# Optimization experiments

Measured on AMD Instinct MI355X. Metric: run time of the kernel, lower is better.

## Reference

```python
import jax, jax.numpy as jnp
import numpy as np

B, T, D, H = 256, 1024, 64, 512
I = 1 + D          # time channel + data
O = 2 * D          # mean + std
STD_LB = 1e-3


def setup_inputs() -> dict:
    key = jax.random.key(0)
    ks = jax.random.split(key, 8)
    s = 0.05  # small init scale
    return {
        "xs": jax.random.normal(ks[0], (B, T, D), jnp.float32),
        "ts": jax.random.uniform(ks[1], (B, T, 1), jnp.float32),
        "W_ih": jax.random.normal(ks[2], (3 * H, I), jnp.float32) * s,
        "W_hh": jax.random.normal(ks[3], (3 * H, H), jnp.float32) * s,
        "b_ih": jax.random.normal(ks[4], (3 * H,), jnp.float32) * s,
        "b_hh": jax.random.normal(ks[5], (3 * H,), jnp.float32) * s,
        "W_dec": jax.random.normal(ks[6], (O, H), jnp.float32) * s,
        "b_dec": jax.random.normal(ks[7], (O,), jnp.float32) * s,
        "cutoff": 512,  # int(inference_start * seq_len) with inference_start=0.5
    }


def reference(xs, ts, W_ih, W_hh, b_ih, b_hh, W_dec, b_dec, cutoff):
    b, t_len, d = xs.shape
    h_dim = W_hh.shape[1]

    def step(carry, inp):
        h, x_hat = carry
        x_true, t_curr, t_idx = inp
        force = t_idx < cutoff  # teacher forcing for t < cutoff
        x_t = jnp.where(force, x_true, x_hat)                 # (B, D)
        x_in = jnp.concatenate([t_curr[:, :1], x_t], axis=-1)  # (B, 1+D)
        gi = x_in @ W_ih.T + b_ih                              # (B, 3H)
        gh = h @ W_hh.T + b_hh                                 # (B, 3H)
        i_r, i_z, i_n = jnp.split(gi, 3, axis=-1)
        h_r, h_z, h_n = jnp.split(gh, 3, axis=-1)
        r = jax.nn.sigmoid(i_r + h_r)
        z = jax.nn.sigmoid(i_z + h_z)
        n = jnp.tanh(i_n + r * h_n)
        h_new = (1.0 - z) * n + z * h                          # GRUCell update
        dec = h_new @ W_dec.T + b_dec                          # (B, 2D)
        mean = dec[:, :d]
        std = jnp.maximum(dec[:, d:], STD_LB)                  # clamp(min=std_lower_bound)
        out = jnp.concatenate([mean, std], axis=-1)
        return (h_new, mean), out

    h0 = jnp.zeros((b, h_dim), xs.dtype)
    init = (h0, xs[:, 0, :])
    xs_t = jnp.swapaxes(xs, 0, 1)   # (T, B, D)
    ts_t = jnp.swapaxes(ts, 0, 1)   # (T, B, 1)
    t_idx = jnp.arange(t_len)
    _, outs = jax.lax.scan(step, init, (xs_t, ts_t, t_idx))
    return jnp.swapaxes(outs, 0, 1)  # (B, T, 2D)
```

## Files before the change

kernel.cpp:

```cpp
#include <hip/hip_runtime.h>
#include <hip/hip_bf16.h>
#include <cstdint>
#include <cstddef>

typedef float f32x4 __attribute__((ext_vector_type(4)));
typedef short s16x8 __attribute__((ext_vector_type(8)));

#define B_  256
#define T_  1024
#define D_  64
#define H_  512
#define O_  128
#define JW  16
#define NG  48

#define SLABW64 49152

#define OFF_WGH   0
#define OFF_WGI2  49152
#define OFF_WGIX  98304
#define OFF_WDEC  104448
#define OFF_W0S   120832
#define OFF_C0S   121024
#define OFF_BIHS  121216
#define OFF_BHHS  121408
#define OFF_BDECS 121600
#define OFF_SCR   121728
#define OFF_SCRF  122752
#define SMEM_BYTES 124928

#define WS_WCOMB 0
#define WS_C0    1572864
#define WS_HSLAB 1579008
#define WS_HSZ   786432

__device__ inline f32x4 mfma16(s16x8 a, s16x8 b, f32x4 c) {
  return __builtin_amdgcn_mfma_f32_16x16x32_bf16(a, b, c, 0, 0, 0);
}

__device__ inline unsigned short f2bf(float f) {
  __hip_bfloat16 h = __float2bfloat16(f);
  unsigned short u;
  __builtin_memcpy(&u, &h, sizeof(u));
  return u;
}

__device__ inline s16x8 cvt8(const float* s) {
  union { unsigned short h[8]; s16x8 v; } p;
#pragma unroll
  for (int e = 0; e < 8; ++e) p.h[e] = f2bf(s[e]);
  return p.v;
}

__device__ inline s16x8 fragK512(const char* base, int n, int kc, int kg) {
  int byteoff = n * 1024 + (((kc * 64) + (kg * 16)) ^ ((n & 7) << 4));
  return *(const s16x8*)(base + byteoff);
}
__device__ inline s16x8 fragK64(const char* base, int n, int kc, int kg) {
  int byteoff = n * 128 + (((kc * 64) + (kg * 16)) ^ ((n & 7) << 4));
  return *(const s16x8*)(base + byteoff);
}

__device__ inline unsigned long long ld64a(const unsigned long long* p) {
  return __hip_atomic_load(p, __ATOMIC_RELAXED, __HIP_MEMORY_SCOPE_AGENT);
}
__device__ inline void st64a(unsigned long long* p, unsigned long long v) {
  __hip_atomic_store(p, v, __ATOMIC_RELAXED, __HIP_MEMORY_SCOPE_AGENT);
}

__device__ inline s16x8 unpack3(unsigned long long w0, unsigned long long w1,
                                unsigned long long w2) {
  union { unsigned short u[8]; s16x8 v; } ua;
  ua.u[0] = (unsigned short)w0; ua.u[1] = (unsigned short)(w0 >> 16);
  ua.u[2] = (unsigned short)(w0 >> 32);
  ua.u[3] = (unsigned short)w1; ua.u[4] = (unsigned short)(w1 >> 16);
  ua.u[5] = (unsigned short)(w1 >> 32);
  ua.u[6] = (unsigned short)w2; ua.u[7] = (unsigned short)(w2 >> 16);
  return ua.v;
}

#define LOADG8(W, KC0)                                                    \
  {                                                                       \
    _Pragma("unroll") for (int k_ = 0; k_ < 8; ++k_) {                    \
      W[k_ * 3 + 0] = ld64a(rqL + ((KC0) + k_) * 192 + 0);                \
      W[k_ * 3 + 1] = ld64a(rqL + ((KC0) + k_) * 192 + 1);                \
      W[k_ * 3 + 2] = ld64a(rqL + ((KC0) + k_) * 192 + 2);                \
    }                                                                     \
  }

#define VERIFY8(W, KC0)                                                   \
  {                                                                       \
    for (;;) {                                                            \
      unsigned long long bad_ = 0;                                        \
      _Pragma("unroll") for (int i_ = 0; i_ < 24; ++i_)                   \
          bad_ |= (W[i_] >> 48) ^ tge;                                    \
      if (!__any((int)(bad_ != 0))) break;                                \
      if (--budget <= 0) break;                                           \
      LOADG8(W, KC0)                                                      \
    }                                                                     \
  }

#define UNPACKG8(W, KC0)                                                  \
  {                                                                       \
    _Pragma("unroll") for (int k_ = 0; k_ < 8; ++k_)                      \
        a[(KC0) + k_] =                                                   \
            unpack3(W[k_ * 3], W[k_ * 3 + 1], W[k_ * 3 + 2]);             \
  }

__global__ void wcomb_kernel(const float* __restrict__ W_ih, const float* __restrict__ W_dec,
                             const float* __restrict__ b_ih, const float* __restrict__ b_dec,
                             unsigned short* __restrict__ Wcomb, float* __restrict__ c0) {
  __shared__ float arow[64];
  int i = blockIdx.x;
  int tid = threadIdx.x;
  if (tid < 64) arow[tid] = W_ih[(size_t)i * 65 + 1 + tid];
  __syncthreads();
  for (int j = tid; j < H_; j += 256) {
    float acc = 0.f;
#pragma unroll 8
    for (int d = 0; d < 64; ++d) acc += arow[d] * W_dec[(size_t)d * H_ + j];
    Wcomb[(size_t)i * H_ + j] = f2bf(acc);
  }
  if (tid == 0) {
    float acc = b_ih[i];
    for (int d = 0; d < 64; ++d) acc += arow[d] * b_dec[d];
    c0[i] = acc;
  }
}

__global__ __launch_bounds__(128, 1) void rnn_persist(
    const float* __restrict__ xs, const float* __restrict__ ts,
    const float* __restrict__ W_ih, const float* __restrict__ W_hh,
    const float* __restrict__ b_ih, const float* __restrict__ b_hh,
    const float* __restrict__ W_dec, const float* __restrict__ b_dec,
    const int* __restrict__ cutoffp,
    const unsigned short* __restrict__ Wcomb, const float* __restrict__ c0,
    unsigned long long* __restrict__ hslabE, float* __restrict__ out) {
  extern __shared__ char sm[];
  const int tid = threadIdx.x;
  const int wave = tid >> 6, lane = tid & 63;
  const int jl = lane & 15, kg = lane >> 4;
  const int cutoff = *cutoffp;

  const int bg = blockIdx.x & 7;
  const int cg = blockIdx.x >> 3;
  const int b0 = bg * 32;
  const int j0 = cg * JW;

  for (int u = tid; u < NG * 64; u += 128) {
    int r = u >> 6, blk = u & 63;
    int grow = (r >> 4) * H_ + j0 + (r & 15);
    s16x8 v = cvt8(W_hh + (size_t)grow * H_ + blk * 8);
    *(s16x8*)(sm + OFF_WGH + r * 1024 + ((blk * 16) ^ ((r & 7) << 4))) = v;
  }
  for (int u = tid; u < NG * 64; u += 128) {
    int r = u >> 6, blk = u & 63;
    int grow = (r >> 4) * H_ + j0 + (r & 15);
    s16x8 v = *(const s16x8*)(Wcomb + (size_t)grow * H_ + blk * 8);
    *(s16x8*)(sm + OFF_WGI2 + r * 1024 + ((blk * 16) ^ ((r & 7) << 4))) = v;
  }
  for (int u = tid; u < NG * 8; u += 128) {
    int r = u >> 3, blk = u & 7;
    int grow = (r >> 4) * H_ + j0 + (r & 15);
    s16x8 v = cvt8(W_ih + (size_t)grow * 65 + 1 + blk * 8);
    *(s16x8*)(sm + OFF_WGIX + r * 128 + ((blk * 16) ^ ((r & 7) << 4))) = v;
  }
  if (cg >= 24) {
    for (int u = tid; u < 16 * 64; u += 128) {
      int r = u >> 6, blk = u & 63;
      s16x8 v = cvt8(W_dec + (size_t)((cg - 24) * 16 + r) * H_ + blk * 8);
      *(s16x8*)(sm + OFF_WDEC + r * 1024 + ((blk * 16) ^ ((r & 7) << 4))) = v;
    }
    if (tid < 16) ((float*)(sm + OFF_BDECS))[tid] = b_dec[(cg - 24) * 16 + tid];
  }
  if (tid < NG) {
    int grow = (tid >> 4) * H_ + j0 + (tid & 15);
    ((float*)(sm + OFF_W0S))[tid]  = W_ih[(size_t)grow * 65];
    ((float*)(sm + OFF_C0S))[tid]  = c0[grow];
    ((float*)(sm + OFF_BIHS))[tid] = b_ih[grow];
    ((float*)(sm + OFF_BHHS))[tid] = b_hh[grow];
  }
  __syncthreads();

  const int mt = wave;
  const int rowg = b0 + mt * 16 + jl;
  const int hrow = b0 + mt * 16 + kg * 4;
  unsigned short* scr = (unsigned short*)(sm + OFF_SCR) + mt * 256;
  float* scrF = (float*)(sm + OFF_SCRF) + mt * 272;
  int budget = 200000;

  const size_t blkb = (size_t)(bg * 2 + mt) * 3072;
  const size_t laneoff = (size_t)kg * 48 + (size_t)jl * 3;
  const int wi0 = lane;
  const int wr0 = wi0 / 6, wk0 = wi0 % 6;
  const int wi1 = 64 + lane;
  const int wr1 = wi1 / 6, wk1 = wi1 % 6;

  const float* W0S  = (const float*)(sm + OFF_W0S);
  const float* C0S  = (const float*)(sm + OFF_C0S);
  const float* BIHS = (const float*)(sm + OFF_BIHS);
  const float* BHHS = (const float*)(sm + OFF_BHHS);
  const float w0r = W0S[jl],  w0z = W0S[16 + jl],  w0n = W0S[32 + jl];
  const float bir = BIHS[jl], biz = BIHS[16 + jl], bin_ = BIHS[32 + jl];
  const float c0r = C0S[jl],  c0z = C0S[16 + jl],  c0n = C0S[32 + jl];
  const float bhr = BHHS[jl], bhz = BHHS[16 + jl], bhn = BHHS[32 + jl];

  const bool do_dec = (cg >= 24);
  const float bd = do_dec ? ((const float*)(sm + OFF_BDECS))[jl] : 0.f;

  float hp[4] = {0.f, 0.f, 0.f, 0.f};
  s16x8 a[16];

  for (int t = 0; t < T_; ++t) {
    const bool use_x = (t < cutoff) || (t == 0);
    const unsigned long long tge = (unsigned long long)(unsigned)t;
    const unsigned long long epw = (unsigned long long)(t + 1) << 48;
    const unsigned long long* rqL =
        hslabE + (size_t)((t + 1) & 1) * SLABW64 + blkb + laneoff;
    unsigned long long* wq = hslabE + (size_t)(t & 1) * SLABW64 + blkb;

    float tsv[4];
#pragma unroll
    for (int reg = 0; reg < 4; ++reg) tsv[reg] = ts[(size_t)(hrow + reg) * T_ + t];

    f32x4 g0{}, g1{}, g2{}, i0{}, i1{}, i2{};
    if (use_x) {
      s16x8 ax0 = cvt8(xs + ((size_t)rowg * T_ + t) * D_ + kg * 8);
      s16x8 ax1 = cvt8(xs + ((size_t)rowg * T_ + t) * D_ + 32 + kg * 8);
      i0 = mfma16(ax0, fragK64(sm + OFF_WGIX, jl,      0, kg), i0);
      i1 = mfma16(ax0, fragK64(sm + OFF_WGIX, 16 + jl, 0, kg), i1);
      i2 = mfma16(ax0, fragK64(sm + OFF_WGIX, 32 + jl, 0, kg), i2);
      i0 = mfma16(ax1, fragK64(sm + OFF_WGIX, jl,      1, kg), i0);
      i1 = mfma16(ax1, fragK64(sm + OFF_WGIX, 16 + jl, 1, kg), i1);
      i2 = mfma16(ax1, fragK64(sm + OFF_WGIX, 32 + jl, 1, kg), i2);
    }

    if (t > 0) {
      unsigned long long wA[24], wB[24];

#define MFMA_CL8(K0)                                                         \
      { _Pragma("unroll") for (int k_ = 0; k_ < 8; ++k_) {                   \
          int kc_ = (K0) + k_;                                               \
          g0 = mfma16(a[kc_], fragK512(sm + OFF_WGH, jl,      kc_, kg), g0); \
          g1 = mfma16(a[kc_], fragK512(sm + OFF_WGH, 16 + jl, kc_, kg), g1); \
          g2 = mfma16(a[kc_], fragK512(sm + OFF_WGH, 32 + jl, kc_, kg), g2); \
          if (!use_x) {                                                      \
            i0 = mfma16(a[kc_], fragK512(sm + OFF_WGI2, jl,      kc_, kg), i0); \
            i1 = mfma16(a[kc_], fragK512(sm + OFF_WGI2, 16 + jl, kc_, kg), i1); \
            i2 = mfma16(a[kc_], fragK512(sm + OFF_WGI2, 32 + jl, kc_, kg), i2); \
          } } }

      LOADG8(wA, 0)
      VERIFY8(wA, 0)
      LOADG8(wB, 8)
      UNPACKG8(wA, 0)
      MFMA_CL8(0)
      VERIFY8(wB, 8)
      UNPACKG8(wB, 8)
      MFMA_CL8(8)
#undef MFMA_CL8
    }

    unsigned short hb[4];
#pragma unroll
    for (int reg = 0; reg < 4; ++reg) {
      const float xr = i0[reg] + tsv[reg] * w0r + (use_x ? bir : c0r) + g0[reg] + bhr;
      const float xz = i1[reg] + tsv[reg] * w0z + (use_x ? biz : c0z) + g1[reg] + bhz;
      const float an = i2[reg] + tsv[reg] * w0n + (use_x ? bin_ : c0n);
      const float gn = g2[reg] + bhn;
      const float r = 1.f / (1.f + __expf(-xr));
      const float z = 1.f / (1.f + __expf(-xz));
      const float e2 = __expf(2.f * (an + r * gn));
      const float n = 1.f - 2.f / (e2 + 1.f);
      const float hn = (1.f - z) * n + z * hp[reg];
      hp[reg] = hn;
      hb[reg] = f2bf(hn);
    }

#pragma unroll
    for (int reg = 0; reg < 4; ++reg) scr[(kg * 4 + reg) * 16 + jl] = hb[reg];
    asm volatile("s_waitcnt lgkmcnt(0)" ::: "memory");
    __builtin_amdgcn_sched_barrier(0);
    {
      const int fg = wk0 / 3, pos = wk0 % 3;
      const int cb = fg * 8 + pos * 3;
      unsigned long long v =
          (unsigned long long)scr[wr0 * 16 + cb] |
          ((unsigned long long)scr[wr0 * 16 + cb + 1] << 16) |
          (pos < 2 ? ((unsigned long long)scr[wr0 * 16 + cb + 2] << 32) : 0ull) |
          epw;
      st64a(wq + (size_t)(cg >> 1) * 192 +
                (size_t)((cg & 1) * 2 + fg) * 48 + (size_t)wr0 * 3 + pos, v);
    }
    if (lane < 32) {
      const int fg = wk1 / 3, pos = wk1 % 3;
      const int cb = fg * 8 + pos * 3;
      unsigned long long v =
          (unsigned long long)scr[wr1 * 16 + cb] |
          ((unsigned long long)scr[wr1 * 16 + cb + 1] << 16) |
          (pos < 2 ? ((unsigned long long)scr[wr1 * 16 + cb + 2] << 32) : 0ull) |
          epw;
      st64a(wq + (size_t)(cg >> 1) * 192 +
                (size_t)((cg & 1) * 2 + fg) * 48 + (size_t)wr1 * 3 + pos, v);
    }

    if (do_dec && t > 0) {
      f32x4 dacc{};
#pragma unroll
      for (int kc = 0; kc < 16; ++kc)
        dacc = mfma16(a[kc], fragK512(sm + OFF_WDEC, jl, kc, kg), dacc);
      const int oc = (cg - 24) * 16 + jl;
#pragma unroll
      for (int reg = 0; reg < 4; ++reg) {
        float vv = dacc[reg] + bd;
        if (oc >= D_) vv = fmaxf(vv, 0.001f);
        scrF[(kg * 4 + reg) * 17 + jl] = vv;
      }
      asm volatile("s_waitcnt lgkmcnt(0)" ::: "memory");
      __builtin_amdgcn_sched_barrier(0);
      {
        const int row = lane >> 2, seg = lane & 3;
        f32x4 ov = *(const f32x4*)(scrF + row * 17 + seg * 4);
        *(f32x4*)(out + ((size_t)(b0 + mt * 16 + row) * T_ + (t - 1)) * O_ +
                  (cg - 24) * 16 + seg * 4) = ov;
      }
    }
  }

  if (do_dec) {
    const unsigned long long tge = (unsigned long long)(unsigned)T_;
    const unsigned long long* rqL =
        hslabE + (size_t)((T_ - 1) & 1) * SLABW64 + blkb + laneoff;
    unsigned long long wA[24], wB[24];
    LOADG8(wA, 0)
    VERIFY8(wA, 0)
    LOADG8(wB, 8)
    UNPACKG8(wA, 0)
    VERIFY8(wB, 8)
    UNPACKG8(wB, 8)
    f32x4 dacc{};
#pragma unroll
    for (int kc = 0; kc < 16; ++kc)
      dacc = mfma16(a[kc], fragK512(sm + OFF_WDEC, jl, kc, kg), dacc);
    const int oc = (cg - 24) * 16 + jl;
#pragma unroll
    for (int reg = 0; reg < 4; ++reg) {
      float vv = dacc[reg] + bd;
      if (oc >= D_) vv = fmaxf(vv, 0.001f);
      scrF[(kg * 4 + reg) * 17 + jl] = vv;
    }
    asm volatile("s_waitcnt lgkmcnt(0)" ::: "memory");
    __builtin_amdgcn_sched_barrier(0);
    {
      const int row = lane >> 2, seg = lane & 3;
      f32x4 ov = *(const f32x4*)(scrF + row * 17 + seg * 4);
      *(f32x4*)(out + ((size_t)(b0 + mt * 16 + row) * T_ + (T_ - 1)) * O_ +
                (cg - 24) * 16 + seg * 4) = ov;
    }
  }
}

extern "C" void kernel_launch(void* const* d_in, const int* in_sizes, int n_in,
                              void* d_out, int out_size, void* d_ws, size_t ws_size,
                              hipStream_t stream) {
  const float* xs    = (const float*)d_in[0];
  const float* ts    = (const float*)d_in[1];
  const float* W_ih  = (const float*)d_in[2];
  const float* W_hh  = (const float*)d_in[3];
  const float* b_ih  = (const float*)d_in[4];
  const float* b_hh  = (const float*)d_in[5];
  const float* W_dec = (const float*)d_in[6];
  const float* b_dec = (const float*)d_in[7];
  const int* cutoff  = (const int*)d_in[8];
  float* out = (float*)d_out;

  char* ws = (char*)d_ws;
  unsigned short* Wcomb      = (unsigned short*)(ws + WS_WCOMB);
  float* c0                  = (float*)(ws + WS_C0);
  unsigned long long* hslabE = (unsigned long long*)(ws + WS_HSLAB);

  hipMemsetAsync(ws + WS_HSLAB, 0, WS_HSZ, stream);
  wcomb_kernel<<<1536, 256, 0, stream>>>(W_ih, W_dec, b_ih, b_dec, Wcomb, c0);
  hipFuncSetAttribute(reinterpret_cast<const void*>(rnn_persist),
                      hipFuncAttributeMaxDynamicSharedMemorySize, SMEM_BYTES);
  rnn_persist<<<256, 128, SMEM_BYTES, stream>>>(xs, ts, W_ih, W_hh, b_ih, b_hh,
                                                W_dec, b_dec, cutoff, Wcomb, c0,
                                                hslabE, out);
}
```

Before: 4.945 ms.

## Move decoder projection to dedicated waves synchronized by progress counters

Blocks now launch with 256 threads. The two extra waves in the first eight column groups act as decoder consumers: each step they read the published hidden state from the global slab, run the output MFMA and write the outputs. Each of these waves publishes a per-wave progress counter. The recurrence waves no longer do decode inline. Instead, before overwriting a double-buffered slab, they spin until the decoder counters have caught up, which takes the decode work off the serial critical path. The scratch row stride is also padded from 16 to 18 to reduce LDS bank conflicts. This adds a cross-wave dependency and spin-wait that could stall the recurrence if the decoder waves fall behind.

```diff
diff --git a/kernel.cpp b/kernel.cpp
--- a/kernel.cpp
+++ b/kernel.cpp
@@ -26,13 +26,15 @@
 #define OFF_BHHS  121408
 #define OFF_BDECS 121600
 #define OFF_SCR   121728
-#define OFF_SCRF  122752
-#define SMEM_BYTES 124928
+#define OFF_SCRF  122880
+#define SMEM_BYTES 125056
 
 #define WS_WCOMB 0
 #define WS_C0    1572864
 #define WS_HSLAB 1579008
 #define WS_HSZ   786432
+#define WS_DPR   2365440
+#define WS_CTL   786944
 
 __device__ inline f32x4 mfma16(s16x8 a, s16x8 b, f32x4 c) {
   return __builtin_amdgcn_mfma_f32_16x16x32_bf16(a, b, c, 0, 0, 0);
@@ -65,6 +67,12 @@
   return __hip_atomic_load(p, __ATOMIC_RELAXED, __HIP_MEMORY_SCOPE_AGENT);
 }
 __device__ inline void st64a(unsigned long long* p, unsigned long long v) {
+  __hip_atomic_store(p, v, __ATOMIC_RELAXED, __HIP_MEMORY_SCOPE_AGENT);
+}
+__device__ inline unsigned ld32a(const unsigned* p) {
+  return __hip_atomic_load(p, __ATOMIC_RELAXED, __HIP_MEMORY_SCOPE_AGENT);
+}
+__device__ inline void st32a(unsigned* p, unsigned v) {
   __hip_atomic_store(p, v, __ATOMIC_RELAXED, __HIP_MEMORY_SCOPE_AGENT);
 }
 
@@ -128,14 +136,15 @@
   }
 }
 
-__global__ __launch_bounds__(128, 1) void rnn_persist(
+__global__ __launch_bounds__(256, 1) void rnn_persist(
     const float* __restrict__ xs, const float* __restrict__ ts,
     const float* __restrict__ W_ih, const float* __restrict__ W_hh,
     const float* __restrict__ b_ih, const float* __restrict__ b_hh,
     const float* __restrict__ W_dec, const float* __restrict__ b_dec,
     const int* __restrict__ cutoffp,
     const unsigned short* __restrict__ Wcomb, const float* __restrict__ c0,
-    unsigned long long* __restrict__ hslabE, float* __restrict__ out) {
+    unsigned long long* __restrict__ hslabE, unsigned* __restrict__ dpr,
+    float* __restrict__ out) {
   extern __shared__ char sm[];
   const int tid = threadIdx.x;
   const int wave = tid >> 6, lane = tid & 63;
@@ -147,31 +156,31 @@
   const int b0 = bg * 32;
   const int j0 = cg * JW;
 
-  for (int u = tid; u < NG * 64; u += 128) {
+  for (int u = tid; u < NG * 64; u += 256) {
     int r = u >> 6, blk = u & 63;
     int grow = (r >> 4) * H_ + j0 + (r & 15);
     s16x8 v = cvt8(W_hh + (size_t)grow * H_ + blk * 8);
     *(s16x8*)(sm + OFF_WGH + r * 1024 + ((blk * 16) ^ ((r & 7) << 4))) = v;
   }
-  for (int u = tid; u < NG * 64; u += 128) {
+  for (int u = tid; u < NG * 64; u += 256) {
     int r = u >> 6, blk = u & 63;
     int grow = (r >> 4) * H_ + j0 + (r & 15);
     s16x8 v = *(const s16x8*)(Wcomb + (size_t)grow * H_ + blk * 8);
     *(s16x8*)(sm + OFF_WGI2 + r * 1024 + ((blk * 16) ^ ((r & 7) << 4))) = v;
   }
-  for (int u = tid; u < NG * 8; u += 128) {
+  for (int u = tid; u < NG * 8; u += 256) {
     int r = u >> 3, blk = u & 7;
     int grow = (r >> 4) * H_ + j0 + (r & 15);
     s16x8 v = cvt8(W_ih + (size_t)grow * 65 + 1 + blk * 8);
     *(s16x8*)(sm + OFF_WGIX + r * 128 + ((blk * 16) ^ ((r & 7) << 4))) = v;
   }
-  if (cg >= 24) {
-    for (int u = tid; u < 16 * 64; u += 128) {
+  if (cg < 8) {
+    for (int u = tid; u < 16 * 64; u += 256) {
       int r = u >> 6, blk = u & 63;
-      s16x8 v = cvt8(W_dec + (size_t)((cg - 24) * 16 + r) * H_ + blk * 8);
+      s16x8 v = cvt8(W_dec + (size_t)(cg * 16 + r) * H_ + blk * 8);
       *(s16x8*)(sm + OFF_WDEC + r * 1024 + ((blk * 16) ^ ((r & 7) << 4))) = v;
     }
-    if (tid < 16) ((float*)(sm + OFF_BDECS))[tid] = b_dec[(cg - 24) * 16 + tid];
+    if (tid < 16) ((float*)(sm + OFF_BDECS))[tid] = b_dec[cg * 16 + tid];
   }
   if (tid < NG) {
     int grow = (tid >> 4) * H_ + j0 + (tid & 15);
@@ -182,12 +191,58 @@
   }
   __syncthreads();
 
+  int budget = 400000;
+
+  if (wave >= 2) {
+    if (cg >= 8) return;
+    const int dmt = wave - 2;
+    const size_t blkb = (size_t)(bg * 2 + dmt) * 3072;
+    const size_t laneoff = (size_t)kg * 48 + (size_t)jl * 3;
+    float* scrF = (float*)(sm + OFF_SCRF) + dmt * 272;
+    const float bd = ((const float*)(sm + OFF_BDECS))[jl];
+    const int oc = cg * 16 + jl;
+    unsigned* myprog = dpr + bg * 16 + cg * 2 + dmt;
+    s16x8 a[16];
+
+    for (int v = 1; v <= T_; ++v) {
+      const unsigned long long tge = (unsigned long long)(unsigned)v;
+      const unsigned long long* rqL =
+          hslabE + (size_t)((v - 1) & 1) * SLABW64 + blkb + laneoff;
+      unsigned long long wA[24], wB[24];
+      LOADG8(wA, 0)
+      VERIFY8(wA, 0)
+      LOADG8(wB, 8)
+      UNPACKG8(wA, 0)
+      VERIFY8(wB, 8)
+      UNPACKG8(wB, 8)
+      if (lane == 0) st32a(myprog, (unsigned)v);
+
+      f32x4 dacc{};
+#pragma unroll
+      for (int kc = 0; kc < 16; ++kc)
+        dacc = mfma16(a[kc], fragK512(sm + OFF_WDEC, jl, kc, kg), dacc);
+#pragma unroll
+      for (int reg = 0; reg < 4; ++reg) {
+        float vv = dacc[reg] + bd;
+        if (oc >= D_) vv = fmaxf(vv, 0.001f);
+        scrF[(kg * 4 + reg) * 17 + jl] = vv;
+      }
+      asm volatile("s_waitcnt lgkmcnt(0)" ::: "memory");
+      __builtin_amdgcn_sched_barrier(0);
+      {
+        const int row = lane >> 2, seg = lane & 3;
+        f32x4 ov = *(const f32x4*)(scrF + row * 17 + seg * 4);
+        *(f32x4*)(out + ((size_t)(b0 + dmt * 16 + row) * T_ + (v - 1)) * O_ +
+                  cg * 16 + seg * 4) = ov;
+      }
+    }
+    return;
+  }
+
   const int mt = wave;
   const int rowg = b0 + mt * 16 + jl;
   const int hrow = b0 + mt * 16 + kg * 4;
-  unsigned short* scr = (unsigned short*)(sm + OFF_SCR) + mt * 256;
-  float* scrF = (float*)(sm + OFF_SCRF) + mt * 272;
-  int budget = 200000;
+  unsigned short* scr = (unsigned short*)(sm + OFF_SCR) + mt * 288;
 
   const size_t blkb = (size_t)(bg * 2 + mt) * 3072;
   const size_t laneoff = (size_t)kg * 48 + (size_t)jl * 3;
@@ -204,9 +259,7 @@
   const float bir = BIHS[jl], biz = BIHS[16 + jl], bin_ = BIHS[32 + jl];
   const float c0r = C0S[jl],  c0z = C0S[16 + jl],  c0n = C0S[32 + jl];
   const float bhr = BHHS[jl], bhz = BHHS[16 + jl], bhn = BHHS[32 + jl];
-
-  const bool do_dec = (cg >= 24);
-  const float bd = do_dec ? ((const float*)(sm + OFF_BDECS))[jl] : 0.f;
+  const unsigned* dprb = dpr + bg * 16;
 
   float hp[4] = {0.f, 0.f, 0.f, 0.f};
   s16x8 a[16];
@@ -218,6 +271,9 @@
     const unsigned long long* rqL =
         hslabE + (size_t)((t + 1) & 1) * SLABW64 + blkb + laneoff;
     unsigned long long* wq = hslabE + (size_t)(t & 1) * SLABW64 + blkb;
+
+    unsigned dv = 0xFFFFFFFFu;
+    if (t >= 2 && lane < 16) dv = ld32a(dprb + lane);
 
     float tsv[4];
 #pragma unroll
@@ -277,17 +333,27 @@
       hb[reg] = f2bf(hn);
     }
 
-#pragma unroll
-    for (int reg = 0; reg < 4; ++reg) scr[(kg * 4 + reg) * 16 + jl] = hb[reg];
+    if (t >= 2) {
+      const unsigned tneed = (unsigned)(t - 1);
+      for (;;) {
+        unsigned v = (lane < 16) ? dv : tneed;
+        if (__all((int)(v >= tneed))) break;
+        if (--budget <= 0) break;
+        if (lane < 16) dv = ld32a(dprb + lane);
+      }
+    }
+
+#pragma unroll
+    for (int reg = 0; reg < 4; ++reg) scr[(kg * 4 + reg) * 18 + jl] = hb[reg];
     asm volatile("s_waitcnt lgkmcnt(0)" ::: "memory");
     __builtin_amdgcn_sched_barrier(0);
     {
       const int fg = wk0 / 3, pos = wk0 % 3;
       const int cb = fg * 8 + pos * 3;
       unsigned long long v =
-          (unsigned long long)scr[wr0 * 16 + cb] |
-          ((unsigned long long)scr[wr0 * 16 + cb + 1] << 16) |
-          (pos < 2 ? ((unsigned long long)scr[wr0 * 16 + cb + 2] << 32) : 0ull) |
+          (unsigned long long)scr[wr0 * 18 + cb] |
+          ((unsigned long long)scr[wr0 * 18 + cb + 1] << 16) |
+          (pos < 2 ? ((unsigned long long)scr[wr0 * 18 + cb + 2] << 32) : 0ull) |
           epw;
       st64a(wq + (size_t)(cg >> 1) * 192 +
                 (size_t)((cg & 1) * 2 + fg) * 48 + (size_t)wr0 * 3 + pos, v);
@@ -296,66 +362,12 @@
       const int fg = wk1 / 3, pos = wk1 % 3;
       const int cb = fg * 8 + pos * 3;
       unsigned long long v =
-          (unsigned long long)scr[wr1 * 16 + cb] |
-          ((unsigned long long)scr[wr1 * 16 + cb + 1] << 16) |
-          (pos < 2 ? ((unsigned long long)scr[wr1 * 16 + cb + 2] << 32) : 0ull) |
+          (unsigned long long)scr[wr1 * 18 + cb] |
+          ((unsigned long long)scr[wr1 * 18 + cb + 1] << 16) |
+          (pos < 2 ? ((unsigned long long)scr[wr1 * 18 + cb + 2] << 32) : 0ull) |
           epw;
       st64a(wq + (size_t)(cg >> 1) * 192 +
                 (size_t)((cg & 1) * 2 + fg) * 48 + (size_t)wr1 * 3 + pos, v);
-    }
-
-    if (do_dec && t > 0) {
-      f32x4 dacc{};
-#pragma unroll
-      for (int kc = 0; kc < 16; ++kc)
-        dacc = mfma16(a[kc], fragK512(sm + OFF_WDEC, jl, kc, kg), dacc);
-      const int oc = (cg - 24) * 16 + jl;
-#pragma unroll
-      for (int reg = 0; reg < 4; ++reg) {
-        float vv = dacc[reg] + bd;
-        if (oc >= D_) vv = fmaxf(vv, 0.001f);
-        scrF[(kg * 4 + reg) * 17 + jl] = vv;
-      }
-      asm volatile("s_waitcnt lgkmcnt(0)" ::: "memory");
-      __builtin_amdgcn_sched_barrier(0);
-      {
-        const int row = lane >> 2, seg = lane & 3;
-        f32x4 ov = *(const f32x4*)(scrF + row * 17 + seg * 4);
-        *(f32x4*)(out + ((size_t)(b0 + mt * 16 + row) * T_ + (t - 1)) * O_ +
-                  (cg - 24) * 16 + seg * 4) = ov;
-      }
-    }
-  }
-
-  if (do_dec) {
-    const unsigned long long tge = (unsigned long long)(unsigned)T_;
-    const unsigned long long* rqL =
-        hslabE + (size_t)((T_ - 1) & 1) * SLABW64 + blkb + laneoff;
-    unsigned long long wA[24], wB[24];
-    LOADG8(wA, 0)
-    VERIFY8(wA, 0)
-    LOADG8(wB, 8)
-    UNPACKG8(wA, 0)
-    VERIFY8(wB, 8)
-    UNPACKG8(wB, 8)
-    f32x4 dacc{};
-#pragma unroll
-    for (int kc = 0; kc < 16; ++kc)
-      dacc = mfma16(a[kc], fragK512(sm + OFF_WDEC, jl, kc, kg), dacc);
-    const int oc = (cg - 24) * 16 + jl;
-#pragma unroll
-    for (int reg = 0; reg < 4; ++reg) {
-      float vv = dacc[reg] + bd;
-      if (oc >= D_) vv = fmaxf(vv, 0.001f);
-      scrF[(kg * 4 + reg) * 17 + jl] = vv;
-    }
-    asm volatile("s_waitcnt lgkmcnt(0)" ::: "memory");
-    __builtin_amdgcn_sched_barrier(0);
-    {
-      const int row = lane >> 2, seg = lane & 3;
-      f32x4 ov = *(const f32x4*)(scrF + row * 17 + seg * 4);
-      *(f32x4*)(out + ((size_t)(b0 + mt * 16 + row) * T_ + (T_ - 1)) * O_ +
-                (cg - 24) * 16 + seg * 4) = ov;
     }
   }
 }
@@ -378,12 +390,13 @@
   unsigned short* Wcomb      = (unsigned short*)(ws + WS_WCOMB);
   float* c0                  = (float*)(ws + WS_C0);
   unsigned long long* hslabE = (unsigned long long*)(ws + WS_HSLAB);
-
-  hipMemsetAsync(ws + WS_HSLAB, 0, WS_HSZ, stream);
+  unsigned* dpr              = (unsigned*)(ws + WS_DPR);
+
+  hipMemsetAsync(ws + WS_HSLAB, 0, WS_CTL, stream);
   wcomb_kernel<<<1536, 256, 0, stream>>>(W_ih, W_dec, b_ih, b_dec, Wcomb, c0);
   hipFuncSetAttribute(reinterpret_cast<const void*>(rnn_persist),
                       hipFuncAttributeMaxDynamicSharedMemorySize, SMEM_BYTES);
-  rnn_persist<<<256, 128, SMEM_BYTES, stream>>>(xs, ts, W_ih, W_hh, b_ih, b_hh,
+  rnn_persist<<<256, 256, SMEM_BYTES, stream>>>(xs, ts, W_ih, W_hh, b_ih, b_hh,
                                                 W_dec, b_dec, cutoff, Wcomb, c0,
-                                                hslabE, out);
-}
+                                                hslabE, dpr, out);
+}
```

Result: slower. 7.177 ms (+45.1%).

## Merge hidden-state poll loops, add sleep backoff, pad scratch stride

Applied to the files above, without the earlier changes.

The per-step spin on the hidden-state slab used to verify each half separately and pipeline the second half's load behind the first half's MFMAs. It now sleeps briefly, loads both halves, and polls them together in one loop before unpacking, which cuts spin traffic on the shared global flag words. The LDS scratch row stride goes from 16 to 18 shorts to reduce bank conflicts, with offsets adjusted to match. In exchange, the first-half MFMAs no longer overlap the second-half load, and the fixed s_sleep adds latency on the serial critical path.

```diff
diff --git a/kernel.cpp b/kernel.cpp
--- a/kernel.cpp
+++ b/kernel.cpp
@@ -13,6 +13,7 @@
 #define O_  128
 #define JW  16
 #define NG  48
+#define SLP 12
 
 #define SLABW64 49152
 
@@ -26,8 +27,8 @@
 #define OFF_BHHS  121408
 #define OFF_BDECS 121600
 #define OFF_SCR   121728
-#define OFF_SCRF  122752
-#define SMEM_BYTES 124928
+#define OFF_SCRF  122880
+#define SMEM_BYTES 125056
 
 #define WS_WCOMB 0
 #define WS_C0    1572864
@@ -88,17 +89,9 @@
     }                                                                     \
   }
 
-#define VERIFY8(W, KC0)                                                   \
-  {                                                                       \
-    for (;;) {                                                            \
-      unsigned long long bad_ = 0;                                        \
-      _Pragma("unroll") for (int i_ = 0; i_ < 24; ++i_)                   \
-          bad_ |= (W[i_] >> 48) ^ tge;                                    \
-      if (!__any((int)(bad_ != 0))) break;                                \
-      if (--budget <= 0) break;                                           \
-      LOADG8(W, KC0)                                                      \
-    }                                                                     \
-  }
+#define BADOF(W) ({ unsigned long long b_ = 0;                            \
+    _Pragma("unroll") for (int i_ = 0; i_ < 24; ++i_)                     \
+        b_ |= (W[i_] >> 48) ^ tge; b_; })
 
 #define UNPACKG8(W, KC0)                                                  \
   {                                                                       \
@@ -185,7 +178,7 @@
   const int mt = wave;
   const int rowg = b0 + mt * 16 + jl;
   const int hrow = b0 + mt * 16 + kg * 4;
-  unsigned short* scr = (unsigned short*)(sm + OFF_SCR) + mt * 256;
+  unsigned short* scr = (unsigned short*)(sm + OFF_SCR) + mt * 288;
   float* scrF = (float*)(sm + OFF_SCRF) + mt * 272;
   int budget = 200000;
 
@@ -237,6 +230,19 @@
 
     if (t > 0) {
       unsigned long long wA[24], wB[24];
+
+      __builtin_amdgcn_s_sleep(SLP);
+      LOADG8(wA, 0)
+      LOADG8(wB, 8)
+      for (;;) {
+        unsigned long long bad = BADOF(wA) | BADOF(wB);
+        if (!__any((int)(bad != 0))) break;
+        if (--budget <= 0) break;
+        LOADG8(wA, 0)
+        LOADG8(wB, 8)
+      }
+      UNPACKG8(wA, 0)
+      UNPACKG8(wB, 8)
 
 #define MFMA_CL8(K0)                                                         \
       { _Pragma("unroll") for (int k_ = 0; k_ < 8; ++k_) {                   \
@@ -250,13 +256,7 @@
             i2 = mfma16(a[kc_], fragK512(sm + OFF_WGI2, 32 + jl, kc_, kg), i2); \
           } } }
 
-      LOADG8(wA, 0)
-      VERIFY8(wA, 0)
-      LOADG8(wB, 8)
-      UNPACKG8(wA, 0)
       MFMA_CL8(0)
-      VERIFY8(wB, 8)
-      UNPACKG8(wB, 8)
       MFMA_CL8(8)
 #undef MFMA_CL8
     }
@@ -278,16 +278,16 @@
     }
 
 #pragma unroll
-    for (int reg = 0; reg < 4; ++reg) scr[(kg * 4 + reg) * 16 + jl] = hb[reg];
+    for (int reg = 0; reg < 4; ++reg) scr[(kg * 4 + reg) * 18 + jl] = hb[reg];
     asm volatile("s_waitcnt lgkmcnt(0)" ::: "memory");
     __builtin_amdgcn_sched_barrier(0);
     {
       const int fg = wk0 / 3, pos = wk0 % 3;
       const int cb = fg * 8 + pos * 3;
       unsigned long long v =
-          (unsigned long long)scr[wr0 * 16 + cb] |
-          ((unsigned long long)scr[wr0 * 16 + cb + 1] << 16) |
-          (pos < 2 ? ((unsigned long long)scr[wr0 * 16 + cb + 2] << 32) : 0ull) |
+          (unsigned long long)scr[wr0 * 18 + cb] |
+          ((unsigned long long)scr[wr0 * 18 + cb + 1] << 16) |
+          (pos < 2 ? ((unsigned long long)scr[wr0 * 18 + cb + 2] << 32) : 0ull) |
           epw;
       st64a(wq + (size_t)(cg >> 1) * 192 +
                 (size_t)((cg & 1) * 2 + fg) * 48 + (size_t)wr0 * 3 + pos, v);
@@ -296,9 +296,9 @@
       const int fg = wk1 / 3, pos = wk1 % 3;
       const int cb = fg * 8 + pos * 3;
       unsigned long long v =
-          (unsigned long long)scr[wr1 * 16 + cb] |
-          ((unsigned long long)scr[wr1 * 16 + cb + 1] << 16) |
-          (pos < 2 ? ((unsigned long long)scr[wr1 * 16 + cb + 2] << 32) : 0ull) |
+          (unsigned long long)scr[wr1 * 18 + cb] |
+          ((unsigned long long)scr[wr1 * 18 + cb + 1] << 16) |
+          (pos < 2 ? ((unsigned long long)scr[wr1 * 18 + cb + 2] << 32) : 0ull) |
           epw;
       st64a(wq + (size_t)(cg >> 1) * 192 +
                 (size_t)((cg & 1) * 2 + fg) * 48 + (size_t)wr1 * 3 + pos, v);
@@ -333,10 +333,15 @@
         hslabE + (size_t)((T_ - 1) & 1) * SLABW64 + blkb + laneoff;
     unsigned long long wA[24], wB[24];
     LOADG8(wA, 0)
-    VERIFY8(wA, 0)
     LOADG8(wB, 8)
+    for (;;) {
+      unsigned long long bad = BADOF(wA) | BADOF(wB);
+      if (!__any((int)(bad != 0))) break;
+      if (--budget <= 0) break;
+      LOADG8(wA, 0)
+      LOADG8(wB, 8)
+    }
     UNPACKG8(wA, 0)
-    VERIFY8(wB, 8)
     UNPACKG8(wB, 8)
     f32x4 dacc{};
 #pragma unroll
```

Result: slower. 5.439 ms (+10.0%).
